# Optimization experiments

Hardware: AMD Instinct MI355X
Metric: run time of the kernel (lower is better)

## Reference

```python
import jax, jax.numpy as jnp
import numpy as np
import math

B, S, DM, H = 2, 2048, 1024, 16
DH = DM // H  # 64


def setup_inputs() -> dict:
    key = jax.random.key(0)
    ks = jax.random.split(key, 12)
    s = 1.0 / math.sqrt(DM)
    inp = {
        "key": jax.random.normal(ks[0], (B, S, DM), jnp.float32),
        "value": jax.random.normal(ks[1], (B, S, DM), jnp.float32),
        "query": jax.random.normal(ks[2], (B, S, DM), jnp.float32),
        # causal mask: True = masked out (matches masked_fill semantics)
        "mask": jnp.broadcast_to(~jnp.tril(jnp.ones((S, S), bool)), (B, S, S)),
        "Wk": jax.random.normal(ks[3], (DM, DM), jnp.float32) * s,
        "bk": jnp.zeros((DM,), jnp.float32),
        "Wv": jax.random.normal(ks[4], (DM, DM), jnp.float32) * s,
        "bv": jnp.zeros((DM,), jnp.float32),
        "Wq": jax.random.normal(ks[5], (DM, DM), jnp.float32) * s,
        "bq": jnp.zeros((DM,), jnp.float32),
        "Wo": jax.random.normal(ks[6], (DM, DM), jnp.float32) * s,
        "bo": jnp.zeros((DM,), jnp.float32),
    }
    return inp


def _split_heads(x):
    # [B, S, H*DH] -> [B, H, S, DH]
    b, s, _ = x.shape
    return x.reshape(b, s, H, DH).transpose(0, 2, 1, 3)


def reference(key, value, query, mask, Wk, bk, Wv, bv, Wq, bq, Wo, bo):
    key_up = _split_heads(key @ Wk.T + bk)      # [B,H,S,DH]
    value_up = _split_heads(value @ Wv.T + bv)  # [B,H,S,DH]
    query_up = _split_heads(query @ Wq.T + bq) / math.sqrt(DH)
    scores = jnp.einsum("bhqd,bhkd->bhqk", query_up, key_up)  # [B,H,S,S]
    scores = jnp.where(mask[:, None, :, :], jnp.float32(-1e18), scores)
    attn = jax.nn.softmax(scores, axis=-1)
    # dropout is identity in eval mode
    context = jnp.einsum("bhqk,bhkd->bhqd", attn, value_up)
    context = context.transpose(0, 2, 1, 3).reshape(key.shape[0], -1, H * DH)
    output = context @ Wo.T + bo                # [B,S,DM]
    top_attn = attn[:, 0, :, :]                 # [B,S,S]
    return output, top_attn
```

## Files before the change

kernel.cpp:

```cpp
#include <hip/hip_runtime.h>
#include <hip/hip_bf16.h>
#include <math.h>

#define B_ 2
#define S_ 2048
#define DM_ 1024
#define H_ 16
#define DH_ 64

using short8 = __attribute__((ext_vector_type(8))) short;
using f32x4  = __attribute__((ext_vector_type(4))) float;

typedef const __attribute__((address_space(1))) void* gas_cvp;
typedef __attribute__((address_space(3))) void* las_vp;

struct CvtJobs {
    const float* in[7];
    ushort* out[7];
};

__device__ __forceinline__ ushort f2bu(float x) {
    __hip_bfloat16 h = __float2bfloat16(x);
    return *(ushort*)&h;
}

__global__ __launch_bounds__(256) void cvt_bf16(CvtJobs jobs) {
    const int bid = blockIdx.x;
    int j, blk;
    if (bid < 6144) { j = bid >> 11; blk = bid & 2047; }
    else { const int r = bid - 6144; j = 3 + (r >> 9); blk = r & 511; }
    const int idx = (blk * 256 + threadIdx.x) * 8;
    const float* in = jobs.in[j];
    float4 a = *(const float4*)&in[idx];
    float4 b = *(const float4*)&in[idx + 4];
    ushort u[8];
    u[0] = f2bu(a.x); u[1] = f2bu(a.y); u[2] = f2bu(a.z); u[3] = f2bu(a.w);
    u[4] = f2bu(b.x); u[5] = f2bu(b.y); u[6] = f2bu(b.z); u[7] = f2bu(b.w);
    *(int4*)&jobs.out[j][idx] = *(int4*)u;
}

struct ProjJobs {
    const ushort* A[3];
    const ushort* W[3];
    const float* bias[3];
    ushort* C[3];
    float scale[3];
};

#define PSTAGE(buf, k0v)                                                       \
    {                                                                          \
        _Pragma("unroll")                                                      \
        for (int i = 0; i < 2; i++) {                                          \
            const int s   = i * 512 + tid;                                     \
            const int c   = s >> 8;                                            \
            const int row = s & 255;                                           \
            __builtin_amdgcn_global_load_lds(                                  \
                (gas_cvp)(Ag + (size_t)(i0 + row) * 1024 + (k0v) + c * 8),     \
                (las_vp)&SH[(buf) * 16384 + (i * 512 + w * 64) * 8], 16, 0, 0);\
            __builtin_amdgcn_global_load_lds(                                  \
                (gas_cvp)(Wg + (size_t)(j0 + row) * 1024 + (k0v) + c * 8),     \
                (las_vp)&SH[(buf) * 16384 + 8192 + (i * 512 + w * 64) * 8],    \
                16, 0, 0);                                                     \
        }                                                                      \
    }

__global__ __launch_bounds__(512) void gemm_proj3(ProjJobs jobs)
{
    __shared__ ushort SH[65536];

    const int o   = blockIdx.x;
    const int swz = (o & 7) * 24 + (o >> 3);
    const int z   = swz >> 6;
    const int rem = swz & 63;
    const int by  = rem >> 2;
    const int bx  = rem & 3;

    const ushort* Ag = jobs.A[z];
    const ushort* Wg = jobs.W[z];
    const float* bias = jobs.bias[z];
    ushort* C = jobs.C[z];
    const float scale = jobs.scale[z];

    const int tid  = threadIdx.x;
    const int w    = tid >> 6;
    const int lane = tid & 63;
    const int g    = lane >> 4;
    const int lr   = lane & 15;
    const int wm   = w >> 2;
    const int wn   = w & 3;
    const int i0   = by * 256;
    const int j0   = bx * 256;

    f32x4 acc[8][4];
    #pragma unroll
    for (int m = 0; m < 8; m++)
        #pragma unroll
        for (int n = 0; n < 4; n++)
            #pragma unroll
            for (int jj = 0; jj < 4; jj++) acc[m][n][jj] = 0.f;

    PSTAGE(0, 0);
    PSTAGE(1, 32);
    PSTAGE(2, 64);

    for (int kt = 0; kt < 32; kt++) {
        if (kt < 30)       asm volatile("s_waitcnt vmcnt(8)" ::: "memory");
        else if (kt == 30) asm volatile("s_waitcnt vmcnt(4)" ::: "memory");
        else               asm volatile("s_waitcnt vmcnt(0)" ::: "memory");
        __builtin_amdgcn_s_barrier();

        if (kt + 3 < 32) PSTAGE((kt + 3) & 3, (kt + 3) * 32);

        const int ab = (kt & 3) * 16384;
        short8 af[8], bf[4];
        #pragma unroll
        for (int m = 0; m < 8; m++)
            af[m] = *(const short8*)&SH[ab + (g * 256 + wm * 128 + m * 16 + lr) * 8];
        #pragma unroll
        for (int n = 0; n < 4; n++)
            bf[n] = *(const short8*)&SH[ab + 8192 + (g * 256 + wn * 64 + n * 16 + lr) * 8];

        __builtin_amdgcn_s_setprio(1);
        #pragma unroll
        for (int m = 0; m < 8; m++)
            #pragma unroll
            for (int n = 0; n < 4; n++)
                acc[m][n] = __builtin_amdgcn_mfma_f32_16x16x32_bf16(
                    af[m], bf[n], acc[m][n], 0, 0, 0);
        __builtin_amdgcn_s_setprio(0);
    }

    const int colbase = j0 + wn * 64;
    const int rowbase = i0 + wm * 128;
    #pragma unroll
    for (int n = 0; n < 4; n++) {
        const int col = colbase + n * 16 + lr;
        const float bb = bias[col];
        const int hh = col >> 6;
        const int d = col & 63;
        #pragma unroll
        for (int m = 0; m < 8; m++) {
            const int rb = rowbase + m * 16 + g * 4;
            #pragma unroll
            for (int jj = 0; jj < 4; jj++) {
                const float v = (acc[m][n][jj] + bb) * scale;
                const int i = rb + jj;
                const int b = i >> 11;
                const int srow = i & 2047;
                C[(((size_t)b * H_ + hh) * S_ + srow) * DH_ + d] = f2bu(v);
            }
        }
    }
}

#define GEMM_STAGE(buf, k0v)                                                   \
    {                                                                          \
        _Pragma("unroll")                                                      \
        for (int i = 0; i < 2; i++) {                                          \
            const int s   = i * 256 + tid;                                     \
            const int c   = s >> 7;                                            \
            const int row = s & 127;                                           \
            __builtin_amdgcn_global_load_lds(                                  \
                (gas_cvp)(Ag + (size_t)(i0 + row) * 1024 + (k0v) + c * 8),     \
                (las_vp)&AsB[buf][0][(i * 256 + w * 64) * 8], 16, 0, 0);       \
            __builtin_amdgcn_global_load_lds(                                  \
                (gas_cvp)(Wg + (size_t)(j0 + row) * 1024 + (k0v) + c * 8),     \
                (las_vp)&AsB[buf][1][(i * 256 + w * 64) * 8], 16, 0, 0);       \
        }                                                                      \
    }

#define GEMM_KLOOP()                                                           \
    {                                                                          \
        int bufc = 0;                                                          \
        GEMM_STAGE(0, 0);                                                      \
        GEMM_STAGE(1, 32);                                                     \
        for (int k0 = 0; k0 < 1024; k0 += 32) {                                \
            if (k0 + 32 < 1024)                                                \
                asm volatile("s_waitcnt vmcnt(4)" ::: "memory");               \
            else                                                               \
                asm volatile("s_waitcnt vmcnt(0)" ::: "memory");               \
            __builtin_amdgcn_s_barrier();                                      \
            if (k0 + 64 < 1024) {                                              \
                const int nb = (bufc + 2 >= 3) ? bufc - 1 : bufc + 2;          \
                GEMM_STAGE(nb, k0 + 64);                                       \
            }                                                                  \
            short8 af[4], bf[4];                                               \
            _Pragma("unroll")                                                  \
            for (int m = 0; m < 4; m++)                                        \
                af[m] = *(const short8*)&AsB[bufc][0][((g << 7) + wm * 64 + m * 16 + lr) * 8]; \
            _Pragma("unroll")                                                  \
            for (int n = 0; n < 4; n++)                                        \
                bf[n] = *(const short8*)&AsB[bufc][1][((g << 7) + wn * 64 + n * 16 + lr) * 8]; \
            _Pragma("unroll")                                                  \
            for (int m = 0; m < 4; m++)                                        \
                _Pragma("unroll")                                              \
                for (int n = 0; n < 4; n++)                                    \
                    acc[m][n] = __builtin_amdgcn_mfma_f32_16x16x32_bf16(       \
                        af[m], bf[n], acc[m][n], 0, 0, 0);                     \
            bufc = (bufc + 1 == 3) ? 0 : bufc + 1;                             \
        }                                                                      \
    }

__global__ __launch_bounds__(256) void flash_mfma(
    const ushort* __restrict__ Qb, const ushort* __restrict__ Kb,
    const ushort* __restrict__ Vb, __hip_bfloat16* __restrict__ ctx,
    float* __restrict__ m0, float* __restrict__ l0)
{
    const int bid = blockIdx.x;
    const int xcd = bid & 7;
    const int t   = bid >> 3;
    const int P   = (t >> 4) * 8 + xcd;
    const int p   = t & 15;
    const int h   = P & 15;
    const int b   = P >> 4;

    const int qtA = p, qtB = 31 - p;
    const size_t hoff = ((size_t)b * H_ + h) * S_ * DH_;
    const ushort* Qh = Qb + hoff;
    const ushort* Kh = Kb + hoff;
    const ushort* Vh = Vb + hoff;

    __shared__ ushort Ks[64][72];
    __shared__ ushort Vt[64][72];
    __shared__ ushort Ps[4][16][72];

    const int tid  = threadIdx.x;
    const int w    = tid >> 6;
    const int lane = tid & 63;
    const int g    = lane >> 4;
    const int lr   = lane & 15;
    const int q0A  = qtA * 64 + w * 16;
    const int q0B  = qtB * 64 + w * 16;

    short8 qfA0, qfA1, qfB0, qfB1;
    {
        const ushort* qa = Qh + (size_t)(q0A + lr) * DH_ + g * 8;
        qfA0 = *(const short8*)(qa);
        qfA1 = *(const short8*)(qa + 32);
        const ushort* qb = Qh + (size_t)(q0B + lr) * DH_ + g * 8;
        qfB0 = *(const short8*)(qb);
        qfB1 = *(const short8*)(qb + 32);
    }

    f32x4 oA[4], oB[4];
    #pragma unroll
    for (int nc = 0; nc < 4; nc++) {
        oA[nc][0]=0.f; oA[nc][1]=0.f; oA[nc][2]=0.f; oA[nc][3]=0.f;
        oB[nc][0]=0.f; oB[nc][1]=0.f; oB[nc][2]=0.f; oB[nc][3]=0.f;
    }
    float mA = -1e30f, lA = 0.f;
    float mB = -1e30f, lB = 0.f;

    const int nkt = qtB + 1;
    const int c0 = w, c1 = w + 4;

    int4 pk0, pk1, pv0, pv1;
    pk0 = *(const int4*)(Kh + (size_t)lane * DH_ + c0 * 8);
    pk1 = *(const int4*)(Kh + (size_t)lane * DH_ + c1 * 8);
    pv0 = *(const int4*)(Vh + (size_t)lane * DH_ + c0 * 8);
    pv1 = *(const int4*)(Vh + (size_t)lane * DH_ + c1 * 8);

    for (int kt = 0; kt < nkt; kt++) {
        const int kvb = kt * 64;
        __syncthreads();
        {
            *(int4*)&Ks[lane][c0 * 8] = pk0;
            *(int4*)&Ks[lane][c1 * 8] = pk1;
            ushort vv[8];
            *(int4*)vv = pv0;
            #pragma unroll
            for (int j2 = 0; j2 < 8; j2++) Vt[c0 * 8 + j2][lane] = vv[j2];
            *(int4*)vv = pv1;
            #pragma unroll
            for (int j2 = 0; j2 < 8; j2++) Vt[c1 * 8 + j2][lane] = vv[j2];
        }
        if (kt + 1 < nkt) {
            const size_t roff = (size_t)(kvb + 64 + lane) * DH_;
            pk0 = *(const int4*)(Kh + roff + c0 * 8);
            pk1 = *(const int4*)(Kh + roff + c1 * 8);
            pv0 = *(const int4*)(Vh + roff + c0 * 8);
            pv1 = *(const int4*)(Vh + roff + c1 * 8);
        }
        __syncthreads();

        #pragma unroll
        for (int u = 0; u < 2; u++) {
            if (u == 0 && kt > qtA) continue;
            const int qt_u  = (u == 0) ? qtA : qtB;
            const int q0w   = (u == 0) ? q0A : q0B;
            const short8 qf0 = (u == 0) ? qfA0 : qfB0;
            const short8 qf1 = (u == 0) ? qfA1 : qfB1;
            float& m_r = (u == 0) ? mA : mB;
            float& l_r = (u == 0) ? lA : lB;
            f32x4* o   = (u == 0) ? oA : oB;
            const int qglob = q0w + lr;

            f32x4 st[4];
            #pragma unroll
            for (int mt = 0; mt < 4; mt++) { st[mt][0]=0.f; st[mt][1]=0.f; st[mt][2]=0.f; st[mt][3]=0.f; }
            __builtin_amdgcn_s_setprio(1);
            #pragma unroll
            for (int mt = 0; mt < 4; mt++) {
                short8 ka = *(const short8*)&Ks[16 * mt + lr][8 * g];
                short8 kb = *(const short8*)&Ks[16 * mt + lr][32 + 8 * g];
                st[mt] = __builtin_amdgcn_mfma_f32_16x16x32_bf16(ka, qf0, st[mt], 0, 0, 0);
                st[mt] = __builtin_amdgcn_mfma_f32_16x16x32_bf16(kb, qf1, st[mt], 0, 0, 0);
            }
            __builtin_amdgcn_s_setprio(0);

            if (kt == qt_u) {
                #pragma unroll
                for (int mt = 0; mt < 4; mt++)
                    #pragma unroll
                    for (int jj = 0; jj < 4; jj++)
                        if (kvb + 16 * mt + 4 * g + jj > qglob) st[mt][jj] = -1e30f;
            }

            float pmax = st[0][0];
            #pragma unroll
            for (int mt = 0; mt < 4; mt++)
                #pragma unroll
                for (int jj = 0; jj < 4; jj++)
                    pmax = fmaxf(pmax, st[mt][jj]);
            pmax = fmaxf(pmax, __shfl_xor(pmax, 16));
            pmax = fmaxf(pmax, __shfl_xor(pmax, 32));

            const bool defer = __all(pmax - m_r <= 8.0f);
            float mnew = m_r, scv = 1.0f;
            if (!defer) {
                mnew = fmaxf(m_r, pmax);
                scv  = __expf(m_r - mnew);
            }

            float lsum = 0.f;
            #pragma unroll
            for (int mt = 0; mt < 4; mt++)
                #pragma unroll
                for (int jj = 0; jj < 4; jj++) {
                    st[mt][jj] = __expf(st[mt][jj] - mnew);
                    lsum += st[mt][jj];
                }
            lsum += __shfl_xor(lsum, 16);
            lsum += __shfl_xor(lsum, 32);
            l_r = l_r * scv + lsum;
            m_r = mnew;

            if (!defer) {
                float sc0 = __shfl(scv, 4 * g + 0);
                float sc1 = __shfl(scv, 4 * g + 1);
                float sc2 = __shfl(scv, 4 * g + 2);
                float sc3 = __shfl(scv, 4 * g + 3);
                #pragma unroll
                for (int nc = 0; nc < 4; nc++) {
                    o[nc][0] *= sc0; o[nc][1] *= sc1;
                    o[nc][2] *= sc2; o[nc][3] *= sc3;
                }
            }

            #pragma unroll
            for (int mt = 0; mt < 4; mt++) {
                ushort u4[4];
                #pragma unroll
                for (int jj = 0; jj < 4; jj++) u4[jj] = f2bu(st[mt][jj]);
                *(uint2*)&Ps[w][lr][16 * mt + 4 * g] = *(uint2*)u4;
            }

            short8 pa0 = *(const short8*)&Ps[w][lr][8 * g];
            short8 pa1 = *(const short8*)&Ps[w][lr][32 + 8 * g];
            __builtin_amdgcn_s_setprio(1);
            #pragma unroll
            for (int nc = 0; nc < 4; nc++) {
                short8 v0 = *(const short8*)&Vt[16 * nc + lr][8 * g];
                short8 v1 = *(const short8*)&Vt[16 * nc + lr][32 + 8 * g];
                o[nc] = __builtin_amdgcn_mfma_f32_16x16x32_bf16(pa0, v0, o[nc], 0, 0, 0);
                o[nc] = __builtin_amdgcn_mfma_f32_16x16x32_bf16(pa1, v1, o[nc], 0, 0, 0);
            }
            __builtin_amdgcn_s_setprio(0);
        }
    }

    #pragma unroll
    for (int u = 0; u < 2; u++) {
        const int q0w = (u == 0) ? q0A : q0B;
        const float m_r = (u == 0) ? mA : mB;
        const float l_r = (u == 0) ? lA : lB;
        const f32x4* o  = (u == 0) ? oA : oB;
        const float linv = 1.0f / l_r;
        float li0 = __shfl(linv, 4 * g + 0);
        float li1 = __shfl(linv, 4 * g + 1);
        float li2 = __shfl(linv, 4 * g + 2);
        float li3 = __shfl(linv, 4 * g + 3);
        #pragma unroll
        for (int reg = 0; reg < 4; reg++) {
            const int qrow = q0w + 4 * g + reg;
            const float li = (reg == 0) ? li0 : (reg == 1) ? li1 : (reg == 2) ? li2 : li3;
            __hip_bfloat16* cp = ctx + ((size_t)b * S_ + qrow) * DM_ + h * DH_;
            #pragma unroll
            for (int nc = 0; nc < 4; nc++)
                cp[16 * nc + lr] = __float2bfloat16(o[nc][reg] * li);
        }
        if (h == 0 && lane < 16) {
            m0[b * S_ + q0w + lane] = m_r;
            l0[b * S_ + q0w + lane] = l_r;
        }
    }
}

__global__ __launch_bounds__(256) void tail_fused(
    const ushort* __restrict__ ctxb, const ushort* __restrict__ Wg_,
    const float* __restrict__ bo, float* __restrict__ out,
    const ushort* __restrict__ Qb, const ushort* __restrict__ Kb,
    const float* __restrict__ m0, const float* __restrict__ l0,
    float* __restrict__ attn)
{
    __shared__ ushort AsB[3][2][4096];
    const int o = blockIdx.x;
    const int tid = threadIdx.x;
    const int w    = tid >> 6;
    const int lane = tid & 63;
    const int g    = lane >> 4;
    const int lr   = lane & 15;

    if (o < 256) {
        const int swz = (o & 7) * 32 + (o >> 3);
        const int by  = swz >> 3;
        const int bx  = swz & 7;
        const int wm  = w >> 1;
        const int wn  = w & 1;
        const int i0  = by * 128;
        const int j0  = bx * 128;
        const ushort* Ag = ctxb;
        const ushort* Wg = Wg_;

        f32x4 acc[4][4];
        #pragma unroll
        for (int m = 0; m < 4; m++)
            #pragma unroll
            for (int n = 0; n < 4; n++)
                #pragma unroll
                for (int jj = 0; jj < 4; jj++) acc[m][n][jj] = 0.f;

        GEMM_KLOOP();

        const int colbase = j0 + wn * 64;
        const int rowbase = i0 + wm * 64;
        #pragma unroll
        for (int n = 0; n < 4; n++) {
            const int col = colbase + n * 16 + lr;
            const float bb = bo[col];
            #pragma unroll
            for (int m = 0; m < 4; m++) {
                const int rb = rowbase + m * 16 + g * 4;
                #pragma unroll
                for (int jj = 0; jj < 4; jj++)
                    out[(size_t)(rb + jj) * DM_ + col] = acc[m][n][jj] + bb;
            }
        }
        return;
    }

    const int t   = o - 256;
    const int kt  = t & 31;
    const int qt2 = (t >> 5) & 31;
    const int b   = t >> 10;
    float* ap = attn + (size_t)b * S_ * S_;

    if (kt > qt2) {
        const int row = qt2 * 64 + (tid >> 2);
        const int col = kt * 64 + (tid & 3) * 16;
        float4 z = {0.f, 0.f, 0.f, 0.f};
        float* rp = ap + (size_t)row * S_ + col;
        *(float4*)&rp[0]  = z;
        *(float4*)&rp[4]  = z;
        *(float4*)&rp[8]  = z;
        *(float4*)&rp[12] = z;
        return;
    }

    ushort (*Ks)[72] = (ushort(*)[72])&AsB[0][0][0];
    const int q0w = qt2 * 64 + w * 16;
    const int kvb = kt * 64;
    const size_t hoff = (size_t)b * H_ * S_ * DH_;
    const ushort* Qh = Qb + hoff;
    const ushort* Kh = Kb + hoff;

    #pragma unroll
    for (int i = 0; i < 2; i++) {
        const int c = w + 4 * i;
        int4 k4 = *(const int4*)(Kh + (size_t)(kvb + lane) * DH_ + c * 8);
        *(int4*)&Ks[lane][c * 8] = k4;
    }

    short8 qf0, qf1;
    {
        const ushort* qp = Qh + (size_t)(q0w + lr) * DH_ + g * 8;
        qf0 = *(const short8*)(qp);
        qf1 = *(const short8*)(qp + 32);
    }
    const int qglob = q0w + lr;
    const float mv   = m0[b * S_ + qglob];
    const float linv = 1.0f / l0[b * S_ + qglob];
    __syncthreads();

    f32x4 st[4];
    #pragma unroll
    for (int mt = 0; mt < 4; mt++) { st[mt][0]=0.f; st[mt][1]=0.f; st[mt][2]=0.f; st[mt][3]=0.f; }
    #pragma unroll
    for (int mt = 0; mt < 4; mt++) {
        short8 ka = *(const short8*)&Ks[16 * mt + lr][8 * g];
        short8 kb = *(const short8*)&Ks[16 * mt + lr][32 + 8 * g];
        st[mt] = __builtin_amdgcn_mfma_f32_16x16x32_bf16(ka, qf0, st[mt], 0, 0, 0);
        st[mt] = __builtin_amdgcn_mfma_f32_16x16x32_bf16(kb, qf1, st[mt], 0, 0, 0);
    }

    float* rowp = ap + (size_t)qglob * S_ + kvb;
    #pragma unroll
    for (int mt = 0; mt < 4; mt++) {
        float4 ov;
        float v[4];
        #pragma unroll
        for (int jj = 0; jj < 4; jj++) {
            const int kv = 16 * mt + 4 * g + jj;
            float pv = __expf(st[mt][jj] - mv) * linv;
            v[jj] = (kvb + kv > qglob) ? 0.f : pv;
        }
        ov.x = v[0]; ov.y = v[1]; ov.z = v[2]; ov.w = v[3];
        *(float4*)&rowp[16 * mt + 4 * g] = ov;
    }
}

extern "C" void kernel_launch(void* const* d_in, const int* in_sizes, int n_in,
                              void* d_out, int out_size, void* d_ws, size_t ws_size,
                              hipStream_t stream)
{
    const float* key   = (const float*)d_in[0];
    const float* value = (const float*)d_in[1];
    const float* query = (const float*)d_in[2];
    const float* Wk = (const float*)d_in[4];
    const float* bk = (const float*)d_in[5];
    const float* Wv = (const float*)d_in[6];
    const float* bv = (const float*)d_in[7];
    const float* Wq = (const float*)d_in[8];
    const float* bq = (const float*)d_in[9];
    const float* Wo = (const float*)d_in[10];
    const float* bo = (const float*)d_in[11];

    char* ws = (char*)d_ws;
    const size_t per = (size_t)B_ * H_ * S_ * DH_;
    const size_t wsz = (size_t)DM_ * DM_;
    __hip_bfloat16* Qp   = (__hip_bfloat16*)ws;
    __hip_bfloat16* Kp   = Qp + per;
    __hip_bfloat16* Vp   = Kp + per;
    __hip_bfloat16* ctxb = Vp + per;
    __hip_bfloat16* qc   = ctxb + per;
    __hip_bfloat16* kc   = qc + per;
    __hip_bfloat16* vc   = kc + per;
    __hip_bfloat16* wqb  = vc + per;
    __hip_bfloat16* wkb  = wqb + wsz;
    __hip_bfloat16* wvb  = wkb + wsz;
    __hip_bfloat16* wob  = wvb + wsz;
    float* m0 = (float*)(wob + wsz);
    float* l0 = m0 + B_ * S_;

    float* out   = (float*)d_out;
    float* topat = out + (size_t)B_ * S_ * DM_;

    CvtJobs jobs;
    jobs.in[0] = query; jobs.out[0] = (ushort*)qc;
    jobs.in[1] = key;   jobs.out[1] = (ushort*)kc;
    jobs.in[2] = value; jobs.out[2] = (ushort*)vc;
    jobs.in[3] = Wq;    jobs.out[3] = (ushort*)wqb;
    jobs.in[4] = Wk;    jobs.out[4] = (ushort*)wkb;
    jobs.in[5] = Wv;    jobs.out[5] = (ushort*)wvb;
    jobs.in[6] = Wo;    jobs.out[6] = (ushort*)wob;
    cvt_bf16<<<6144 + 4 * 512, 256, 0, stream>>>(jobs);

    ProjJobs pj;
    pj.A[0] = (const ushort*)qc; pj.W[0] = (const ushort*)wqb; pj.bias[0] = bq;
    pj.C[0] = (ushort*)Qp; pj.scale[0] = 0.125f;
    pj.A[1] = (const ushort*)kc; pj.W[1] = (const ushort*)wkb; pj.bias[1] = bk;
    pj.C[1] = (ushort*)Kp; pj.scale[1] = 1.0f;
    pj.A[2] = (const ushort*)vc; pj.W[2] = (const ushort*)wvb; pj.bias[2] = bv;
    pj.C[2] = (ushort*)Vp; pj.scale[2] = 1.0f;
    gemm_proj3<<<192, 512, 0, stream>>>(pj);

    flash_mfma<<<512, 256, 0, stream>>>(
        (const ushort*)Qp, (const ushort*)Kp, (const ushort*)Vp, ctxb, m0, l0);

    tail_fused<<<256 + B_ * 32 * 32, 256, 0, stream>>>(
        (const ushort*)ctxb, (const ushort*)wob, bo, out,
        (const ushort*)Qp, (const ushort*)Kp, m0, l0, topat);
}
```

Measured before the change: 154.6 us.

## Split projection GEMM staging into halves and use 512-thread flash blocks

The projection GEMM now issues the A-tile and W-tile prefetches in two separate phases, each placed after the LDS reads for that part of the k-step. The MFMA work is split into two halves with an extra barrier between them, so global-to-LDS traffic is spread across the compute. The flash attention kernel moves from 256-thread blocks on 64-row query tiles to 512-thread blocks on 128-row tile pairs, with per-wave diagonal tracking and one K/V load per thread. This halves the block count and shares each K/V tile across more query rows, but adds a barrier per k-step and more per-block LDS and causal imbalance within a block.

Measured after the change: 139.0 us. 1.11x faster.

```diff
diff --git a/kernel.cpp b/kernel.cpp
--- a/kernel.cpp
+++ b/kernel.cpp
@@ -47,7 +47,7 @@
     float scale[3];
 };
 
-#define PSTAGE(buf, k0v)                                                       \
+#define PSTAGE_A(buf, k0v)                                                     \
     {                                                                          \
         _Pragma("unroll")                                                      \
         for (int i = 0; i < 2; i++) {                                          \
@@ -57,6 +57,16 @@
             __builtin_amdgcn_global_load_lds(                                  \
                 (gas_cvp)(Ag + (size_t)(i0 + row) * 1024 + (k0v) + c * 8),     \
                 (las_vp)&SH[(buf) * 16384 + (i * 512 + w * 64) * 8], 16, 0, 0);\
+        }                                                                      \
+    }
+
+#define PSTAGE_B(buf, k0v)                                                     \
+    {                                                                          \
+        _Pragma("unroll")                                                      \
+        for (int i = 0; i < 2; i++) {                                          \
+            const int s   = i * 512 + tid;                                     \
+            const int c   = s >> 8;                                            \
+            const int row = s & 255;                                           \
             __builtin_amdgcn_global_load_lds(                                  \
                 (gas_cvp)(Wg + (size_t)(j0 + row) * 1024 + (k0v) + c * 8),     \
                 (las_vp)&SH[(buf) * 16384 + 8192 + (i * 512 + w * 64) * 8],    \
@@ -99,9 +109,9 @@
             #pragma unroll
             for (int jj = 0; jj < 4; jj++) acc[m][n][jj] = 0.f;
 
-    PSTAGE(0, 0);
-    PSTAGE(1, 32);
-    PSTAGE(2, 64);
+    PSTAGE_A(0, 0);  PSTAGE_B(0, 0);
+    PSTAGE_A(1, 32); PSTAGE_B(1, 32);
+    PSTAGE_A(2, 64); PSTAGE_B(2, 64);
 
     for (int kt = 0; kt < 32; kt++) {
         if (kt < 30)       asm volatile("s_waitcnt vmcnt(8)" ::: "memory");
@@ -109,24 +119,40 @@
         else               asm volatile("s_waitcnt vmcnt(0)" ::: "memory");
         __builtin_amdgcn_s_barrier();
 
-        if (kt + 3 < 32) PSTAGE((kt + 3) & 3, (kt + 3) * 32);
-
         const int ab = (kt & 3) * 16384;
-        short8 af[8], bf[4];
+
+        short8 af[8], bf01[2];
         #pragma unroll
         for (int m = 0; m < 8; m++)
             af[m] = *(const short8*)&SH[ab + (g * 256 + wm * 128 + m * 16 + lr) * 8];
         #pragma unroll
-        for (int n = 0; n < 4; n++)
-            bf[n] = *(const short8*)&SH[ab + 8192 + (g * 256 + wn * 64 + n * 16 + lr) * 8];
+        for (int n = 0; n < 2; n++)
+            bf01[n] = *(const short8*)&SH[ab + 8192 + (g * 256 + wn * 64 + n * 16 + lr) * 8];
+        if (kt + 3 < 32) PSTAGE_A((kt + 3) & 3, (kt + 3) * 32);
 
         __builtin_amdgcn_s_setprio(1);
         #pragma unroll
         for (int m = 0; m < 8; m++)
             #pragma unroll
-            for (int n = 0; n < 4; n++)
+            for (int n = 0; n < 2; n++)
                 acc[m][n] = __builtin_amdgcn_mfma_f32_16x16x32_bf16(
-                    af[m], bf[n], acc[m][n], 0, 0, 0);
+                    af[m], bf01[n], acc[m][n], 0, 0, 0);
+        __builtin_amdgcn_s_setprio(0);
+        __builtin_amdgcn_s_barrier();
+
+        short8 bf23[2];
+        #pragma unroll
+        for (int n = 0; n < 2; n++)
+            bf23[n] = *(const short8*)&SH[ab + 8192 + (g * 256 + wn * 64 + (n + 2) * 16 + lr) * 8];
+        if (kt + 3 < 32) PSTAGE_B((kt + 3) & 3, (kt + 3) * 32);
+
+        __builtin_amdgcn_s_setprio(1);
+        #pragma unroll
+        for (int m = 0; m < 8; m++)
+            #pragma unroll
+            for (int n = 0; n < 2; n++)
+                acc[m][n + 2] = __builtin_amdgcn_mfma_f32_16x16x32_bf16(
+                    af[m], bf23[n], acc[m][n + 2], 0, 0, 0);
         __builtin_amdgcn_s_setprio(0);
     }
 
@@ -201,7 +227,7 @@
         }                                                                      \
     }
 
-__global__ __launch_bounds__(256) void flash_mfma(
+__global__ __launch_bounds__(512) void flash_mfma(
     const ushort* __restrict__ Qb, const ushort* __restrict__ Kb,
     const ushort* __restrict__ Vb, __hip_bfloat16* __restrict__ ctx,
     float* __restrict__ m0, float* __restrict__ l0)
@@ -209,12 +235,11 @@
     const int bid = blockIdx.x;
     const int xcd = bid & 7;
     const int t   = bid >> 3;
-    const int P   = (t >> 4) * 8 + xcd;
-    const int p   = t & 15;
+    const int P   = (t >> 3) * 8 + xcd;
+    const int p   = t & 7;
     const int h   = P & 15;
     const int b   = P >> 4;
 
-    const int qtA = p, qtB = 31 - p;
     const size_t hoff = ((size_t)b * H_ + h) * S_ * DH_;
     const ushort* Qh = Qb + hoff;
     const ushort* Kh = Kb + hoff;
@@ -222,15 +247,18 @@
 
     __shared__ ushort Ks[64][72];
     __shared__ ushort Vt[64][72];
-    __shared__ ushort Ps[4][16][72];
+    __shared__ ushort Ps[8][16][72];
 
     const int tid  = threadIdx.x;
     const int w    = tid >> 6;
     const int lane = tid & 63;
     const int g    = lane >> 4;
     const int lr   = lane & 15;
-    const int q0A  = qtA * 64 + w * 16;
-    const int q0B  = qtB * 64 + w * 16;
+    const int q0A  = p * 128 + w * 16;
+    const int q0B  = (15 - p) * 128 + w * 16;
+    const int diagA = (q0A + 15) >> 6;
+    const int diagB = (q0B + 15) >> 6;
+    const int nkt   = 2 * (16 - p);
 
     short8 qfA0, qfA1, qfB0, qfB1;
     {
@@ -251,42 +279,30 @@
     float mA = -1e30f, lA = 0.f;
     float mB = -1e30f, lB = 0.f;
 
-    const int nkt = qtB + 1;
-    const int c0 = w, c1 = w + 4;
-
-    int4 pk0, pk1, pv0, pv1;
-    pk0 = *(const int4*)(Kh + (size_t)lane * DH_ + c0 * 8);
-    pk1 = *(const int4*)(Kh + (size_t)lane * DH_ + c1 * 8);
-    pv0 = *(const int4*)(Vh + (size_t)lane * DH_ + c0 * 8);
-    pv1 = *(const int4*)(Vh + (size_t)lane * DH_ + c1 * 8);
+    int4 pk = *(const int4*)(Kh + (size_t)lane * DH_ + w * 8);
+    int4 pv = *(const int4*)(Vh + (size_t)lane * DH_ + w * 8);
 
     for (int kt = 0; kt < nkt; kt++) {
         const int kvb = kt * 64;
         __syncthreads();
         {
-            *(int4*)&Ks[lane][c0 * 8] = pk0;
-            *(int4*)&Ks[lane][c1 * 8] = pk1;
+            *(int4*)&Ks[lane][w * 8] = pk;
             ushort vv[8];
-            *(int4*)vv = pv0;
-            #pragma unroll
-            for (int j2 = 0; j2 < 8; j2++) Vt[c0 * 8 + j2][lane] = vv[j2];
-            *(int4*)vv = pv1;
-            #pragma unroll
-            for (int j2 = 0; j2 < 8; j2++) Vt[c1 * 8 + j2][lane] = vv[j2];
+            *(int4*)vv = pv;
+            #pragma unroll
+            for (int j2 = 0; j2 < 8; j2++) Vt[w * 8 + j2][lane] = vv[j2];
         }
         if (kt + 1 < nkt) {
-            const size_t roff = (size_t)(kvb + 64 + lane) * DH_;
-            pk0 = *(const int4*)(Kh + roff + c0 * 8);
-            pk1 = *(const int4*)(Kh + roff + c1 * 8);
-            pv0 = *(const int4*)(Vh + roff + c0 * 8);
-            pv1 = *(const int4*)(Vh + roff + c1 * 8);
+            const size_t roff = (size_t)(kvb + 64 + lane) * DH_ + w * 8;
+            pk = *(const int4*)(Kh + roff);
+            pv = *(const int4*)(Vh + roff);
         }
         __syncthreads();
 
         #pragma unroll
         for (int u = 0; u < 2; u++) {
-            if (u == 0 && kt > qtA) continue;
-            const int qt_u  = (u == 0) ? qtA : qtB;
+            const int diag = (u == 0) ? diagA : diagB;
+            if (kt > diag) continue;
             const int q0w   = (u == 0) ? q0A : q0B;
             const short8 qf0 = (u == 0) ? qfA0 : qfB0;
             const short8 qf1 = (u == 0) ? qfA1 : qfB1;
@@ -308,7 +324,7 @@
             }
             __builtin_amdgcn_s_setprio(0);
 
-            if (kt == qt_u) {
+            if (kt == diag) {
                 #pragma unroll
                 for (int mt = 0; mt < 4; mt++)
                     #pragma unroll
@@ -584,7 +600,7 @@
     pj.C[2] = (ushort*)Vp; pj.scale[2] = 1.0f;
     gemm_proj3<<<192, 512, 0, stream>>>(pj);
 
-    flash_mfma<<<512, 256, 0, stream>>>(
+    flash_mfma<<<256, 512, 0, stream>>>(
         (const ushort*)Qp, (const ushort*)Kp, (const ushort*)Vp, ctxb, m0, l0);
 
     tail_fused<<<256 + B_ * 32 * 32, 256, 0, stream>>>(
```
